# Performance work log

Measured on AMD Instinct MI355X. Metric: run time of the kernel, lower is better.

Reference implementation:

```python
import jax, jax.numpy as jnp
import numpy as np

N = 4_000_000      # total rows across all strata
D = 64             # covariate dimension (nn.Linear input_size)
N_SEG = 100_000    # number of strata (groups)


def setup_inputs() -> dict:
    key = jax.random.key(0)
    k1, k2, k3, k4 = jax.random.split(key, 4)
    X = jax.random.normal(k1, (N, D), dtype=jnp.float32)
    # sorted segment ids encode the ragged strata lengths (rows are packed per group)
    seg_ids = jnp.sort(jax.random.randint(k2, (N,), 0, N_SEG)).astype(jnp.int32)
    w = jax.random.normal(k3, (D,), dtype=jnp.float32) * 0.1
    b = jax.random.normal(k4, (1,), dtype=jnp.float32)
    return {"X": X, "seg_ids": seg_ids, "w": w, "b": b}


def reference(X, seg_ids, w, b):
    # linear projection to a single logit per row: y_hat = X @ w + b
    logits = X @ w + b[0]                                   # [N]
    # segment softmax == padded (-300) row softmax with padding underflowing to 0
    m = jax.ops.segment_max(logits, seg_ids, num_segments=N_SEG)   # [N_SEG]
    m = jnp.where(jnp.isfinite(m), m, jnp.float32(0.0))            # guard empty segments
    z = jnp.exp(logits - m[seg_ids])                               # [N]
    denom = jax.ops.segment_sum(z, seg_ids, num_segments=N_SEG)    # [N_SEG]
    return z / denom[seg_ids]                                      # [N] per-group softmax probs
```

## Files before the change

kernel.cpp:

```cpp
#include <hip/hip_runtime.h>
#include <math.h>

#define NROWS 4000000
#define DCOV  64
#define NSEG  100000

#define SEGS_PER_BLOCK 25
#define NBLOCKS (NSEG / SEGS_PER_BLOCK)
#define CAP 2048

typedef float f32x4 __attribute__((ext_vector_type(4)));

__device__ __forceinline__ int lower_bound_seg(const int* __restrict__ seg,
                                               int target, int lane) {
    int lo = 0, n = NROWS;
    while (n > 64) {
        const int step = (n + 63) >> 6;
        const long long p = (long long)lo + (long long)(lane + 1) * step;
        const bool lt = (p < (long long)lo + n) && (seg[p] < target);
        const int cnt = (int)__popcll(__ballot(lt));
        lo += cnt * step;
        n = min(step, n - cnt * step);
    }
    const bool lt = (lane < n) && (seg[lo + lane] < target);
    return lo + (int)__popcll(__ballot(lt));
}

__global__ __launch_bounds__(256, 8)
void fused_clr_kernel(const float* __restrict__ X,
                      const int* __restrict__ seg,
                      const float* __restrict__ w,
                      const float* __restrict__ b,
                      float* __restrict__ out,
                      float* __restrict__ gl ) {
    __shared__ int   st_lds[SEGS_PER_BLOCK + 1];
    __shared__ float logit_lds[CAP];
    __shared__ int   rs_sh, re_sh;

    const int tid  = threadIdx.x;
    const int lane = tid & 63;
    const int wv   = tid >> 6;
    const int sub  = lane & 15;
    const int rig  = lane >> 4;

    const int s0 = blockIdx.x * SEGS_PER_BLOCK;
    const int s1 = s0 + SEGS_PER_BLOCK;

    if (wv == 0) {
        int r = lower_bound_seg(seg, s0, lane);
        if (lane == 0) rs_sh = r;
    } else if (wv == 1) {
        int r = lower_bound_seg(seg, s1, lane);
        if (lane == 0) re_sh = r;
    }
    __syncthreads();
    const int row_start = rs_sh;
    const int row_end   = re_sh;
    const int nrows     = row_end - row_start;

    const bool  use_lds = (nrows <= CAP);
    const float bias    = b[0];
    const float4 w4     = reinterpret_cast<const float4*>(w)[sub];
    const f32x4* Xv     = reinterpret_cast<const f32x4*>(X);

    if (nrows == 0) {
        if (tid <= SEGS_PER_BLOCK) st_lds[tid] = row_end;
    } else {
        for (int i = row_start + tid; i < row_end; i += 256) {
            const int s    = seg[i];
            const int prev = (i == row_start) ? (s0 - 1) : seg[i - 1];
            for (int t = prev + 1; t <= s; ++t) st_lds[t - s0] = i;
            if (i == row_end - 1) {
                for (int t = s + 1; t <= s1; ++t) st_lds[t - s0] = row_end;
            }
        }
    }

    for (int rb = row_start + wv * 16; rb < row_end; rb += 64) {
        const int r0 = rb + rig, r1 = rb + 4 + rig, r2 = rb + 8 + rig, r3 = rb + 12 + rig;
        f32x4 x0 = {0,0,0,0}, x1 = {0,0,0,0}, x2 = {0,0,0,0}, x3 = {0,0,0,0};
        const f32x4* xp = Xv + (long long)rb * 16 + lane;
        if (r0 < row_end) x0 = __builtin_nontemporal_load(xp);
        if (r1 < row_end) x1 = __builtin_nontemporal_load(xp + 64);
        if (r2 < row_end) x2 = __builtin_nontemporal_load(xp + 128);
        if (r3 < row_end) x3 = __builtin_nontemporal_load(xp + 192);
        float p0 = x0.x * w4.x + x0.y * w4.y + x0.z * w4.z + x0.w * w4.w;
        float p1 = x1.x * w4.x + x1.y * w4.y + x1.z * w4.z + x1.w * w4.w;
        float p2 = x2.x * w4.x + x2.y * w4.y + x2.z * w4.z + x2.w * w4.w;
        float p3 = x3.x * w4.x + x3.y * w4.y + x3.z * w4.z + x3.w * w4.w;
        #pragma unroll
        for (int m = 1; m < 16; m <<= 1) {
            p0 += __shfl_xor(p0, m);
            p1 += __shfl_xor(p1, m);
            p2 += __shfl_xor(p2, m);
            p3 += __shfl_xor(p3, m);
        }
        if (sub == 0) {
            if (use_lds) {
                if (r0 < row_end) logit_lds[r0 - row_start] = p0 + bias;
                if (r1 < row_end) logit_lds[r1 - row_start] = p1 + bias;
                if (r2 < row_end) logit_lds[r2 - row_start] = p2 + bias;
                if (r3 < row_end) logit_lds[r3 - row_start] = p3 + bias;
            } else {
                if (r0 < row_end) gl[r0] = p0 + bias;
                if (r1 < row_end) gl[r1] = p1 + bias;
                if (r2 < row_end) gl[r2] = p2 + bias;
                if (r3 < row_end) gl[r3] = p3 + bias;
            }
        }
    }
    __syncthreads();

    for (int j = wv; j < SEGS_PER_BLOCK; j += 4) {
        const int a0  = st_lds[j];
        const int a1  = st_lds[j + 1];
        const int len = a1 - a0;
        if (len <= 0) continue;
        if (len <= 64) {
            const bool act = lane < len;
            const int  idx = a0 - row_start + lane;
            float x = act ? (use_lds ? logit_lds[idx] : gl[a0 + lane]) : -INFINITY;
            float mx = x;
            #pragma unroll
            for (int m = 1; m < 64; m <<= 1) mx = fmaxf(mx, __shfl_xor(mx, m));
            float e = act ? __expf(x - mx) : 0.0f;
            float sum = e;
            #pragma unroll
            for (int m = 1; m < 64; m <<= 1) sum += __shfl_xor(sum, m);
            if (act) __builtin_nontemporal_store(e / sum, &out[a0 + lane]);
        } else {
            float mx = -INFINITY;
            for (int i = a0 + lane; i < a1; i += 64)
                mx = fmaxf(mx, use_lds ? logit_lds[i - row_start] : gl[i]);
            #pragma unroll
            for (int m = 1; m < 64; m <<= 1) mx = fmaxf(mx, __shfl_xor(mx, m));
            float sum = 0.0f;
            for (int i = a0 + lane; i < a1; i += 64)
                sum += __expf((use_lds ? logit_lds[i - row_start] : gl[i]) - mx);
            #pragma unroll
            for (int m = 1; m < 64; m <<= 1) sum += __shfl_xor(sum, m);
            const float inv = 1.0f / sum;
            for (int i = a0 + lane; i < a1; i += 64) {
                float pr = __expf((use_lds ? logit_lds[i - row_start] : gl[i]) - mx) * inv;
                __builtin_nontemporal_store(pr, &out[i]);
            }
        }
    }
}

extern "C" void kernel_launch(void* const* d_in, const int* in_sizes, int n_in,
                              void* d_out, int out_size, void* d_ws, size_t ws_size,
                              hipStream_t stream) {
    const float* X   = (const float*)d_in[0];
    const int*   seg = (const int*)d_in[1];
    const float* w   = (const float*)d_in[2];
    const float* b   = (const float*)d_in[3];
    float*       out = (float*)d_out;
    float*       gl  = (float*)d_ws;

    fused_clr_kernel<<<NBLOCKS, 256, 0, stream>>>(X, seg, w, b, out, gl);
}
```

Measured before the change: 183.3 us.

## Make each wavefront own its segment range and drop block-wide barriers

Each wave now independently binary-searches its own 8-segment row range, computes the logits into a per-wave LDS slice and runs the softmax, so the block-level __syncthreads calls are gone. The goal is to remove barrier stalls and the load imbalance that came from sharing one row range across four waves. In exchange every wave runs two binary searches instead of two per block, and there is less parallelism per segment range. The missing block barrier relies on wave-synchronous LDS visibility, with only a fence on the global-fallback path.

```diff
diff --git a/kernel.cpp b/kernel.cpp
--- a/kernel.cpp
+++ b/kernel.cpp
@@ -5,9 +5,11 @@
 #define DCOV  64
 #define NSEG  100000
 
-#define SEGS_PER_BLOCK 25
-#define NBLOCKS (NSEG / SEGS_PER_BLOCK)
-#define CAP 2048
+#define SEGS_PER_WAVE   8
+#define WAVES_PER_BLOCK 4
+#define SEGS_PER_BLOCK  (SEGS_PER_WAVE * WAVES_PER_BLOCK)
+#define NBLOCKS         (NSEG / SEGS_PER_BLOCK)
+#define WCAP            1024
 
 typedef float f32x4 __attribute__((ext_vector_type(4)));
 
@@ -33,9 +35,8 @@
                       const float* __restrict__ b,
                       float* __restrict__ out,
                       float* __restrict__ gl ) {
-    __shared__ int   st_lds[SEGS_PER_BLOCK + 1];
-    __shared__ float logit_lds[CAP];
-    __shared__ int   rs_sh, re_sh;
+    __shared__ float logit_lds[WAVES_PER_BLOCK][WCAP];
+    __shared__ int   st_lds[WAVES_PER_BLOCK][SEGS_PER_WAVE + 1];
 
     const int tid  = threadIdx.x;
     const int lane = tid & 63;
@@ -43,40 +44,36 @@
     const int sub  = lane & 15;
     const int rig  = lane >> 4;
 
-    const int s0 = blockIdx.x * SEGS_PER_BLOCK;
-    const int s1 = s0 + SEGS_PER_BLOCK;
+    const int gw  = blockIdx.x * WAVES_PER_BLOCK + wv;
+    const int ws0 = gw * SEGS_PER_WAVE;
+    const int ws1 = ws0 + SEGS_PER_WAVE;
 
-    if (wv == 0) {
-        int r = lower_bound_seg(seg, s0, lane);
-        if (lane == 0) rs_sh = r;
-    } else if (wv == 1) {
-        int r = lower_bound_seg(seg, s1, lane);
-        if (lane == 0) re_sh = r;
-    }
-    __syncthreads();
-    const int row_start = rs_sh;
-    const int row_end   = re_sh;
+    float* __restrict__ wlds = logit_lds[wv];
+    int*   __restrict__ wst  = st_lds[wv];
+
+    const int row_start = lower_bound_seg(seg, ws0, lane);
+    const int row_end   = lower_bound_seg(seg, ws1, lane);
     const int nrows     = row_end - row_start;
 
-    const bool  use_lds = (nrows <= CAP);
+    const bool  use_lds = (nrows <= WCAP);
     const float bias    = b[0];
     const float4 w4     = reinterpret_cast<const float4*>(w)[sub];
     const f32x4* Xv     = reinterpret_cast<const f32x4*>(X);
 
     if (nrows == 0) {
-        if (tid <= SEGS_PER_BLOCK) st_lds[tid] = row_end;
+        if (lane <= SEGS_PER_WAVE) wst[lane] = row_end;
     } else {
-        for (int i = row_start + tid; i < row_end; i += 256) {
+        for (int i = row_start + lane; i < row_end; i += 64) {
             const int s    = seg[i];
-            const int prev = (i == row_start) ? (s0 - 1) : seg[i - 1];
-            for (int t = prev + 1; t <= s; ++t) st_lds[t - s0] = i;
+            const int prev = (i == row_start) ? (ws0 - 1) : seg[i - 1];
+            for (int t = prev + 1; t <= s; ++t) wst[t - ws0] = i;
             if (i == row_end - 1) {
-                for (int t = s + 1; t <= s1; ++t) st_lds[t - s0] = row_end;
+                for (int t = s + 1; t <= ws1; ++t) wst[t - ws0] = row_end;
             }
         }
     }
 
-    for (int rb = row_start + wv * 16; rb < row_end; rb += 64) {
+    for (int rb = row_start; rb < row_end; rb += 16) {
         const int r0 = rb + rig, r1 = rb + 4 + rig, r2 = rb + 8 + rig, r3 = rb + 12 + rig;
         f32x4 x0 = {0,0,0,0}, x1 = {0,0,0,0}, x2 = {0,0,0,0}, x3 = {0,0,0,0};
         const f32x4* xp = Xv + (long long)rb * 16 + lane;
@@ -97,10 +94,10 @@
         }
         if (sub == 0) {
             if (use_lds) {
-                if (r0 < row_end) logit_lds[r0 - row_start] = p0 + bias;
-                if (r1 < row_end) logit_lds[r1 - row_start] = p1 + bias;
-                if (r2 < row_end) logit_lds[r2 - row_start] = p2 + bias;
-                if (r3 < row_end) logit_lds[r3 - row_start] = p3 + bias;
+                if (r0 < row_end) wlds[r0 - row_start] = p0 + bias;
+                if (r1 < row_end) wlds[r1 - row_start] = p1 + bias;
+                if (r2 < row_end) wlds[r2 - row_start] = p2 + bias;
+                if (r3 < row_end) wlds[r3 - row_start] = p3 + bias;
             } else {
                 if (r0 < row_end) gl[r0] = p0 + bias;
                 if (r1 < row_end) gl[r1] = p1 + bias;
@@ -109,17 +106,17 @@
             }
         }
     }
-    __syncthreads();
+    if (!use_lds) __threadfence_block();
 
-    for (int j = wv; j < SEGS_PER_BLOCK; j += 4) {
-        const int a0  = st_lds[j];
-        const int a1  = st_lds[j + 1];
+    for (int j = 0; j < SEGS_PER_WAVE; ++j) {
+        const int a0  = wst[j];
+        const int a1  = wst[j + 1];
         const int len = a1 - a0;
         if (len <= 0) continue;
         if (len <= 64) {
             const bool act = lane < len;
             const int  idx = a0 - row_start + lane;
-            float x = act ? (use_lds ? logit_lds[idx] : gl[a0 + lane]) : -INFINITY;
+            float x = act ? (use_lds ? wlds[idx] : gl[a0 + lane]) : -INFINITY;
             float mx = x;
             #pragma unroll
             for (int m = 1; m < 64; m <<= 1) mx = fmaxf(mx, __shfl_xor(mx, m));
@@ -131,17 +128,17 @@
         } else {
             float mx = -INFINITY;
             for (int i = a0 + lane; i < a1; i += 64)
-                mx = fmaxf(mx, use_lds ? logit_lds[i - row_start] : gl[i]);
+                mx = fmaxf(mx, use_lds ? wlds[i - row_start] : gl[i]);
             #pragma unroll
             for (int m = 1; m < 64; m <<= 1) mx = fmaxf(mx, __shfl_xor(mx, m));
             float sum = 0.0f;
             for (int i = a0 + lane; i < a1; i += 64)
-                sum += __expf((use_lds ? logit_lds[i - row_start] : gl[i]) - mx);
+                sum += __expf((use_lds ? wlds[i - row_start] : gl[i]) - mx);
             #pragma unroll
             for (int m = 1; m < 64; m <<= 1) sum += __shfl_xor(sum, m);
             const float inv = 1.0f / sum;
             for (int i = a0 + lane; i < a1; i += 64) {
-                float pr = __expf((use_lds ? logit_lds[i - row_start] : gl[i]) - mx) * inv;
+                float pr = __expf((use_lds ? wlds[i - row_start] : gl[i]) - mx) * inv;
                 __builtin_nontemporal_store(pr, &out[i]);
             }
         }
```

Result: slower. 199.7 us (+8.9%).
